# Kernel optimization log

Measured on AMD Instinct MI355X. Metric: run time of the kernel, lower is better.

The kernel has to match this reference:

```python
import jax, jax.numpy as jnp
import numpy as np

# Cross-attention fusion core (SpatialTransformer CrossAttention, LDM-style):
#   q = x @ Wq ; k = ctx @ Wk ; v = ctx @ Wv  (bias-free projections)
#   multi-head split, sim = q k^T * d_head**-0.5, softmax, out = attn v, merge heads, to_out.

N_HEADS = 2
D_HEAD = 32


def setup_inputs() -> dict:
    key = jax.random.key(0)
    ks = jax.random.split(key, 7)
    B, N, C = 8, 3136, 64           # batch=bs*num_key, tokens=H*W=56*56, snn channels
    Nc, Cc = 3136, 64               # ann context tokens / channels (resnet18 layer1)
    inner = N_HEADS * D_HEAD        # 64
    std = 0.02
    return {
        "x": jax.random.normal(ks[0], (B, N, C), jnp.float32),
        "context": jax.random.normal(ks[1], (B, Nc, Cc), jnp.float32),
        "Wq": std * jax.random.normal(ks[2], (C, inner), jnp.float32),
        "Wk": std * jax.random.normal(ks[3], (Cc, inner), jnp.float32),
        "Wv": std * jax.random.normal(ks[4], (Cc, inner), jnp.float32),
        "Wo": std * jax.random.normal(ks[5], (inner, C), jnp.float32),
        "bo": jnp.zeros((C,), jnp.float32),
    }


def reference(x, context, Wq, Wk, Wv, Wo, bo):
    B, N, C = x.shape
    H, D = N_HEADS, D_HEAD
    scale = D ** -0.5
    # projections -> [B, H, N, D]
    q = jnp.einsum('bnc,ci->bni', x, Wq).reshape(B, N, H, D).transpose(0, 2, 1, 3)
    k = jnp.einsum('bmc,ci->bmi', context, Wk).reshape(B, -1, H, D).transpose(0, 2, 1, 3)
    v = jnp.einsum('bmc,ci->bmi', context, Wv).reshape(B, -1, H, D).transpose(0, 2, 1, 3)
    # full attention matrix [B, H, N, Nc] (as in the original explicit-einsum impl)
    sim = jnp.einsum('bhid,bhjd->bhij', q, k) * scale
    attn = jax.nn.softmax(sim, axis=-1)
    out = jnp.einsum('bhij,bhjd->bhid', attn, v)
    out = out.transpose(0, 2, 1, 3).reshape(B, N, H * D)
    return jnp.einsum('bni,ic->bnc', out, Wo) + bo
```

## Files before the change

### kernel.cpp

```cpp
#include <hip/hip_runtime.h>
#include <hip/hip_bf16.h>


constexpr int Bc = 8;
constexpr int Nq = 3136;
constexpr int NT = 49;
constexpr size_t SEG   = (size_t)Bc * Nq * 64;
constexpr size_t OPOFF = 3 * SEG;
constexpr size_t LPOFF = OPOFF + (size_t)1176 * 4096;
constexpr size_t WS_NEED3 = (LPOFF + (size_t)1176 * 256) * 2;

typedef short bf16x8 __attribute__((ext_vector_type(8)));
typedef float f32x4  __attribute__((ext_vector_type(4)));

#define QSCALE (0.17677669529663687f * 1.4426950408889634f)

__device__ inline unsigned int f2bf(float f) {
    __hip_bfloat16 h = __float2bfloat16(f);
    unsigned short u;
    __builtin_memcpy(&u, &h, 2);
    return (unsigned int)u;
}

__device__ inline unsigned int cvtpk(float lo, float hi) {
    unsigned int r;
    asm("v_cvt_pk_bf16_f32 %0, %1, %2" : "=v"(r) : "v"(lo), "v"(hi));
    return r;
}

__device__ inline float exp2_hw(float x) { return __builtin_amdgcn_exp2f(x); }

#define GLOAD16(gp, lp)                                                        \
    __builtin_amdgcn_global_load_lds(                                          \
        (const __attribute__((address_space(1))) unsigned int*)(gp),           \
        (__attribute__((address_space(3))) unsigned int*)(lp), 16, 0, 0)

__global__ __launch_bounds__(256)
void proj_kernel(const float* __restrict__ x, const float* __restrict__ ctx,
                 const float* __restrict__ Wq, const float* __restrict__ Wk,
                 const float* __restrict__ Wv, unsigned short* __restrict__ ws) {
    __shared__ short Xls[128 * 72];
    __shared__ short Wtl[64 * 72];

    const int m = blockIdx.y;
    const float* in = (m == 0) ? x : ctx;
    const float* W  = (m == 0) ? Wq : (m == 1 ? Wk : Wv);
    const size_t row0 = (size_t)blockIdx.x * 128;
    const int tid = threadIdx.x;

    {
        const int k  = tid & 63;
        const int cb = tid >> 6;
        const float* wr = W + k * 64 + cb * 16;
        float4 w0 = *(const float4*)(wr + 0);
        float4 w1 = *(const float4*)(wr + 4);
        float4 w2 = *(const float4*)(wr + 8);
        float4 w3 = *(const float4*)(wr + 12);
        float wv[16] = {w0.x,w0.y,w0.z,w0.w, w1.x,w1.y,w1.z,w1.w,
                        w2.x,w2.y,w2.z,w2.w, w3.x,w3.y,w3.z,w3.w};
#pragma unroll
        for (int j = 0; j < 16; ++j)
            Wtl[(cb * 16 + j) * 72 + k] = (short)f2bf(wv[j]);
    }
    {
        const int r    = tid >> 1;
        const int half = tid & 1;
        const float* xr = in + (row0 + r) * 64 + half * 32;
        unsigned int u[16];
#pragma unroll
        for (int i = 0; i < 8; ++i) {
            float4 v = *(const float4*)(xr + 4 * i);
            u[2*i]   = f2bf(v.x) | (f2bf(v.y) << 16);
            u[2*i+1] = f2bf(v.z) | (f2bf(v.w) << 16);
        }
        char* dst = (char*)Xls + r * 144 + half * 64;
#pragma unroll
        for (int c = 0; c < 4; ++c)
            *(uint4*)(dst + 16 * c) = make_uint4(u[4*c], u[4*c+1], u[4*c+2], u[4*c+3]);
    }
    __syncthreads();

    const int lane = tid & 63;
    const int w    = tid >> 6;
    const int l15  = lane & 15;
    const int g    = lane >> 4;

    f32x4 acc[2][4];
#pragma unroll
    for (int ti = 0; ti < 2; ++ti)
#pragma unroll
        for (int tc = 0; tc < 4; ++tc) acc[ti][tc] = (f32x4){0.f,0.f,0.f,0.f};

#pragma unroll
    for (int kk = 0; kk < 2; ++kk) {
#pragma unroll
        for (int ti = 0; ti < 2; ++ti) {
            const int T = 2 * w + ti;
            bf16x8 a = *(const bf16x8*)((char*)Xls + (16 * T + l15) * 144 + kk * 64 + 16 * g);
#pragma unroll
            for (int tc = 0; tc < 4; ++tc) {
                bf16x8 bfr = *(const bf16x8*)((char*)Wtl + (16 * tc + l15) * 144 + kk * 64 + 16 * g);
                acc[ti][tc] = __builtin_amdgcn_mfma_f32_16x16x32_bf16(a, bfr, acc[ti][tc], 0, 0, 0);
            }
        }
    }

    unsigned short* Qs = ws;
    char* Ktc = (char*)(ws + SEG);
    char* Vtc = (char*)(ws + 2 * SEG);

#pragma unroll
    for (int ti = 0; ti < 2; ++ti) {
#pragma unroll
        for (int tc = 0; tc < 4; ++tc) {
            const int col = 16 * tc + l15;
            if (m == 0) {
#pragma unroll
                for (int r = 0; r < 4; ++r) {
                    const size_t grow = row0 + 32 * w + 16 * ti + 4 * g + r;
                    Qs[grow * 64 + col] = (unsigned short)f2bf(acc[ti][tc][r] * QSCALE);
                }
            } else if (m == 1) {
#pragma unroll
                for (int r = 0; r < 4; ++r) {
                    const size_t grow = row0 + 32 * w + 16 * ti + 4 * g + r;
                    const size_t tile = grow >> 6;
                    const int key = (int)(grow & 63);
                    const int off = (key * 128 + col * 2) ^ ((key & 7) << 4);
                    *(unsigned short*)(Ktc + tile * 8192 + off) =
                        (unsigned short)f2bf(acc[ti][tc][r]);
                }
            } else {
                const size_t grow0 = row0 + 32 * w + 16 * ti + 4 * g;
                const size_t tile = grow0 >> 6;
                const int key0 = (int)(grow0 & 63);
                const int off = (col * 128 + key0 * 2) ^ ((col & 15) << 3);
                uint2 pv;
                pv.x = f2bf(acc[ti][tc][0]) | (f2bf(acc[ti][tc][1]) << 16);
                pv.y = f2bf(acc[ti][tc][2]) | (f2bf(acc[ti][tc][3]) << 16);
                *(uint2*)(Vtc + tile * 8192 + off) = pv;
            }
        }
    }
}

__global__ __launch_bounds__(256)
void flash_kernel(unsigned short* __restrict__ ws, int P) {
    __shared__ __align__(16) char pool[32768];
    char* Kpool = pool;
    char* Vpool = pool + 16384;

    const int tid   = threadIdx.x;
    const int lane  = tid & 63;
    const int w     = tid >> 6;
    const int h     = w & 1;
    const int half  = w >> 1;
    const int l15   = lane & 15;
    const int g     = lane >> 4;
    const int bid   = blockIdx.x;
    const int b     = bid & 7;
    const int idx   = bid >> 3;
    const int qt    = idx / P;
    const int part  = idx - qt * P;
    const int q0    = qt * 64;
    const int base  = NT / P, rem = NT - base * P;
    const int t0    = part * base + (part < rem ? part : rem);
    const int tend  = t0 + base + (part < rem ? 1 : 0);

    const unsigned short* Qs = ws;
    const char* Ktb = (const char*)(ws + SEG)     + (size_t)b * NT * 8192;
    const char* Vtb = (const char*)(ws + 2 * SEG) + (size_t)b * NT * 8192;

    const unsigned short* qp0 =
        Qs + ((size_t)(b * Nq + q0 + half * 32 + l15)) * 64 + h * 32 + g * 8;
    const bf16x8 qf0 = *(const bf16x8*)qp0;
    const bf16x8 qf1 = *(const bf16x8*)(qp0 + 16 * 64);

    const int koff  = (l15 * 128 + h * 64 + g * 16) ^ ((l15 & 7) << 4);
    const int vrowA = (h * 32 + l15) * 128;
    const int vsw   = l15 << 3;
    const int stoff = tid * 16;

    union VF { bf16x8 v; unsigned int u[4]; };
    VF ones;
    ones.u[0] = 0x3F803F80u; ones.u[1] = 0x3F803F80u;
    ones.u[2] = 0x3F803F80u; ones.u[3] = 0x3F803F80u;

    f32x4 oacc00 = {0.f,0.f,0.f,0.f};
    f32x4 oacc01 = {0.f,0.f,0.f,0.f};
    f32x4 oacc10 = {0.f,0.f,0.f,0.f};
    f32x4 oacc11 = {0.f,0.f,0.f,0.f};
    f32x4 ls0    = {0.f,0.f,0.f,0.f};
    f32x4 ls1    = {0.f,0.f,0.f,0.f};

#pragma unroll
    for (int i = 0; i < 2; ++i) {
        const char* ks = Ktb + (size_t)(t0 + i) * 8192;
        const char* vs = Vtb + (size_t)(t0 + i) * 8192;
        GLOAD16(ks + stoff,        Kpool + i * 8192 + stoff);
        GLOAD16(ks + stoff + 4096, Kpool + i * 8192 + stoff + 4096);
        GLOAD16(vs + stoff,        Vpool + i * 8192 + stoff);
        GLOAD16(vs + stoff + 4096, Vpool + i * 8192 + stoff + 4096);
    }
    asm volatile("s_waitcnt vmcnt(4)" ::: "memory");
    __builtin_amdgcn_s_barrier();
    __builtin_amdgcn_sched_barrier(0);

#pragma unroll 1
    for (int t = t0; t < tend; ++t) {
        const int cb = (t - t0) & 1;
        const char* Kb = Kpool + cb * 8192;
        const char* Vb = Vpool + cb * 8192;

        __builtin_amdgcn_s_setprio(1);
        bf16x8 kA0 = *(const bf16x8*)(Kb + koff);
        bf16x8 kA1 = *(const bf16x8*)(Kb + 2048 + koff);
        bf16x8 kB0 = *(const bf16x8*)(Kb + 4096 + koff);
        bf16x8 kB1 = *(const bf16x8*)(Kb + 4096 + 2048 + koff);
        uint2 vA00 = *(const uint2*)(Vb + ((vrowA +       8 * g) ^ vsw));
        uint2 vA01 = *(const uint2*)(Vb + ((vrowA + 32 +  8 * g) ^ vsw));
        uint2 vA10 = *(const uint2*)(Vb + ((vrowA + 2048 +      8 * g) ^ vsw));
        uint2 vA11 = *(const uint2*)(Vb + ((vrowA + 2048 + 32 + 8 * g) ^ vsw));
        uint2 vB00 = *(const uint2*)(Vb + ((vrowA + 64 +      8 * g) ^ vsw));
        uint2 vB01 = *(const uint2*)(Vb + ((vrowA + 64 + 32 + 8 * g) ^ vsw));
        uint2 vB10 = *(const uint2*)(Vb + ((vrowA + 2048 + 64 +      8 * g) ^ vsw));
        uint2 vB11 = *(const uint2*)(Vb + ((vrowA + 2048 + 64 + 32 + 8 * g) ^ vsw));

#define CHUNK(kf0, kf1, v00, v01, v10, v11)                                     \
        {                                                                       \
            f32x4 s0a = __builtin_amdgcn_mfma_f32_16x16x32_bf16(kf0, qf0, (f32x4){0.f,0.f,0.f,0.f}, 0, 0, 0); \
            f32x4 s1a = __builtin_amdgcn_mfma_f32_16x16x32_bf16(kf1, qf0, (f32x4){0.f,0.f,0.f,0.f}, 0, 0, 0); \
            f32x4 s0b = __builtin_amdgcn_mfma_f32_16x16x32_bf16(kf0, qf1, (f32x4){0.f,0.f,0.f,0.f}, 0, 0, 0); \
            f32x4 s1b = __builtin_amdgcn_mfma_f32_16x16x32_bf16(kf1, qf1, (f32x4){0.f,0.f,0.f,0.f}, 0, 0, 0); \
            float pa0 = exp2_hw(s0a[0]), pa1 = exp2_hw(s0a[1]);                 \
            float pa2 = exp2_hw(s0a[2]), pa3 = exp2_hw(s0a[3]);                 \
            float pa4 = exp2_hw(s1a[0]), pa5 = exp2_hw(s1a[1]);                 \
            float pa6 = exp2_hw(s1a[2]), pa7 = exp2_hw(s1a[3]);                 \
            float pb0 = exp2_hw(s0b[0]), pb1 = exp2_hw(s0b[1]);                 \
            float pb2 = exp2_hw(s0b[2]), pb3 = exp2_hw(s0b[3]);                 \
            float pb4 = exp2_hw(s1b[0]), pb5 = exp2_hw(s1b[1]);                 \
            float pb6 = exp2_hw(s1b[2]), pb7 = exp2_hw(s1b[3]);                 \
            VF af0, af1;                                                        \
            af0.u[0] = cvtpk(pa0, pa1); af0.u[1] = cvtpk(pa2, pa3);             \
            af0.u[2] = cvtpk(pa4, pa5); af0.u[3] = cvtpk(pa6, pa7);             \
            af1.u[0] = cvtpk(pb0, pb1); af1.u[1] = cvtpk(pb2, pb3);             \
            af1.u[2] = cvtpk(pb4, pb5); af1.u[3] = cvtpk(pb6, pb7);             \
            VF vfA, vfB;                                                        \
            vfA.u[0] = v00.x; vfA.u[1] = v00.y; vfA.u[2] = v01.x; vfA.u[3] = v01.y; \
            vfB.u[0] = v10.x; vfB.u[1] = v10.y; vfB.u[2] = v11.x; vfB.u[3] = v11.y; \
            oacc00 = __builtin_amdgcn_mfma_f32_16x16x32_bf16(af0.v, vfA.v, oacc00, 0, 0, 0); \
            oacc01 = __builtin_amdgcn_mfma_f32_16x16x32_bf16(af0.v, vfB.v, oacc01, 0, 0, 0); \
            oacc10 = __builtin_amdgcn_mfma_f32_16x16x32_bf16(af1.v, vfA.v, oacc10, 0, 0, 0); \
            oacc11 = __builtin_amdgcn_mfma_f32_16x16x32_bf16(af1.v, vfB.v, oacc11, 0, 0, 0); \
            ls0    = __builtin_amdgcn_mfma_f32_16x16x32_bf16(af0.v, ones.v, ls0, 0, 0, 0);   \
            ls1    = __builtin_amdgcn_mfma_f32_16x16x32_bf16(af1.v, ones.v, ls1, 0, 0, 0);   \
        }

        CHUNK(kA0, kA1, vA00, vA01, vA10, vA11)
        CHUNK(kB0, kB1, vB00, vB01, vB10, vB11)
#undef CHUNK
        __builtin_amdgcn_s_setprio(0);

        if (t + 1 < tend) {
            __builtin_amdgcn_s_barrier();
            __builtin_amdgcn_sched_barrier(0);
            if (t + 2 < tend) {
                const char* ks = Ktb + (size_t)(t + 2) * 8192;
                const char* vs = Vtb + (size_t)(t + 2) * 8192;
                GLOAD16(ks + stoff,        Kb + stoff);
                GLOAD16(ks + stoff + 4096, Kb + stoff + 4096);
                GLOAD16(vs + stoff,        Vb + stoff);
                GLOAD16(vs + stoff + 4096, Vb + stoff + 4096);
                asm volatile("s_waitcnt vmcnt(4)" ::: "memory");
            } else {
                asm volatile("s_waitcnt vmcnt(0)" ::: "memory");
            }
            __builtin_amdgcn_s_barrier();
            __builtin_amdgcn_sched_barrier(0);
        }
    }

    float* lp = (float*)(ws + LPOFF) + (size_t)bid * 128;
    if (l15 == 0) {
#pragma unroll
        for (int r = 0; r < 4; ++r) {
            lp[h * 64 + half * 32 + 4 * g + r]      = ls0[r];
            lp[h * 64 + half * 32 + 16 + 4 * g + r] = ls1[r];
        }
    }

    _Float16* Op = (_Float16*)(ws + OPOFF) + (size_t)bid * 4096;
#pragma unroll
    for (int r = 0; r < 4; ++r) {
        const int q = half * 32 + 4 * g + r;
        Op[q * 64 + h * 32 + l15]             = (_Float16)oacc00[r];
        Op[q * 64 + h * 32 + 16 + l15]        = (_Float16)oacc01[r];
        Op[(q + 16) * 64 + h * 32 + l15]      = (_Float16)oacc10[r];
        Op[(q + 16) * 64 + h * 32 + 16 + l15] = (_Float16)oacc11[r];
    }
}

__global__ __launch_bounds__(256)
void combine_kernel(const unsigned short* __restrict__ ws, const float* __restrict__ Wo,
                    const float* __restrict__ bo, float* __restrict__ out, int P) {
    __shared__ short As[64 * 72];
    __shared__ short Wtl[64 * 72];

    const int tid = threadIdx.x;
    const int cid = blockIdx.x;
    const int b   = cid & 7;
    const int qt  = cid >> 3;
    const int q0  = qt * 64;

    const int bid0 = ((qt * P) << 3) | b;

    {
        const int k  = tid & 63;
        const int cb = tid >> 6;
        const float* wr = Wo + k * 64 + cb * 16;
        float4 w0 = *(const float4*)(wr + 0);
        float4 w1 = *(const float4*)(wr + 4);
        float4 w2 = *(const float4*)(wr + 8);
        float4 w3 = *(const float4*)(wr + 12);
        float wv[16] = {w0.x,w0.y,w0.z,w0.w, w1.x,w1.y,w1.z,w1.w,
                        w2.x,w2.y,w2.z,w2.w, w3.x,w3.y,w3.z,w3.w};
#pragma unroll
        for (int j = 0; j < 16; ++j)
            Wtl[(cb * 16 + j) * 72 + k] = (short)f2bf(wv[j]);
    }

    {
        const int r  = tid >> 2;
        const int cg = (tid & 3) << 4;
        const int hh = cg >> 5;

        float lsum = 0.f;
        float o[16];
#pragma unroll
        for (int j = 0; j < 16; ++j) o[j] = 0.f;

        for (int p = 0; p < P; ++p) {
            const int pb = bid0 + 8 * p;
            const float* lpp = (const float*)(ws + LPOFF) + (size_t)pb * 128;
            lsum += lpp[hh * 64 + r];
            const _Float16* Opp = (const _Float16*)(ws + OPOFF) + (size_t)pb * 4096;
            union H4 { uint4 u; _Float16 h[8]; };
            H4 x0, x1;
            x0.u = *(const uint4*)(Opp + (size_t)r * 64 + cg);
            x1.u = *(const uint4*)(Opp + (size_t)r * 64 + cg + 8);
#pragma unroll
            for (int j = 0; j < 8; ++j) {
                o[j]     += (float)x0.h[j];
                o[j + 8] += (float)x1.h[j];
            }
        }
        const float inv = 1.0f / lsum;
        short* arow = As + r * 72 + cg;
#pragma unroll
        for (int j = 0; j < 16; ++j) arow[j] = (short)f2bf(o[j] * inv);
    }
    __syncthreads();

    const int lane = tid & 63;
    const int w    = tid >> 6;
    const int l15  = lane & 15;
    const int g    = lane >> 4;
#pragma unroll
    for (int tc = 0; tc < 4; ++tc) {
        const int col = 16 * tc + l15;
        const float bias = bo[col];
        f32x4 accE = {bias, bias, bias, bias};
#pragma unroll
        for (int kk = 0; kk < 2; ++kk) {
            bf16x8 a   = *(const bf16x8*)((char*)As  + (16 * w + l15) * 144 + kk * 64 + 16 * g);
            bf16x8 bfr = *(const bf16x8*)((char*)Wtl + col * 144 + kk * 64 + 16 * g);
            accE = __builtin_amdgcn_mfma_f32_16x16x32_bf16(a, bfr, accE, 0, 0, 0);
        }
        float* ob = out + ((size_t)(b * Nq + q0 + 16 * w + 4 * g)) * 64 + col;
#pragma unroll
        for (int r = 0; r < 4; ++r) ob[(size_t)r * 64] = accE[r];
    }
}

extern "C" void kernel_launch(void* const* d_in, const int* in_sizes, int n_in,
                              void* d_out, int out_size, void* d_ws, size_t ws_size,
                              hipStream_t stream) {
    const float* x   = (const float*)d_in[0];
    const float* ctx = (const float*)d_in[1];
    const float* Wq  = (const float*)d_in[2];
    const float* Wk  = (const float*)d_in[3];
    const float* Wv  = (const float*)d_in[4];
    const float* Wo  = (const float*)d_in[5];
    const float* bo  = (const float*)d_in[6];
    float* out = (float*)d_out;
    unsigned short* ws = (unsigned short*)d_ws;

    const int P = (ws_size >= WS_NEED3) ? 3 : 2;

    dim3 gproj(Bc * Nq / 128, 3);
    proj_kernel<<<gproj, 256, 0, stream>>>(x, ctx, Wq, Wk, Wv, ws);

    flash_kernel<<<dim3(Nq / 64 * Bc * P), 256, 0, stream>>>(ws, P);

    combine_kernel<<<dim3(Nq / 64 * Bc), 256, 0, stream>>>(ws, Wo, bo, out, P);
}
```

Measured before the change: 57.41 us.

## Switch flash inner loop to 32x32x16 MFMA with VALU row sums

Replaces the 16x16x32 MFMA tiling in the attention loop with 32x32x16 bf16 MFMAs, so each wave computes a 32-key by 32-query score tile and a 32x32 output tile. The V tile layout written by the projection kernel is re-swizzled to match the new operand fragments. The softmax denominator is now accumulated with VALU adds plus a cross-half shuffle instead of extra MFMAs against a ones vector. This aims to cut MFMA issue count and per-tile LDS reads, at the cost of a larger 16-wide accumulator and dependence on the new swizzle being correct.

New measurement: 62.05 us. +8.1%, slower.

```diff
diff --git a/kernel.cpp b/kernel.cpp
--- a/kernel.cpp
+++ b/kernel.cpp
@@ -12,6 +12,8 @@
 
 typedef short bf16x8 __attribute__((ext_vector_type(8)));
 typedef float f32x4  __attribute__((ext_vector_type(4)));
+typedef float f32x16 __attribute__((ext_vector_type(16)));
+typedef float f32x2  __attribute__((ext_vector_type(2)));
 
 #define QSCALE (0.17677669529663687f * 1.4426950408889634f)
 
@@ -134,7 +136,10 @@
                 const size_t grow0 = row0 + 32 * w + 16 * ti + 4 * g;
                 const size_t tile = grow0 >> 6;
                 const int key0 = (int)(grow0 & 63);
-                const int off = (col * 128 + key0 * 2) ^ ((col & 15) << 3);
+                const int kb = (key0 >> 2) & 3;
+                const int sb = ((kb & 1) << 1) | (kb >> 1);
+                const int off = (col * 128 + (key0 >> 4) * 32 + sb * 8)
+                                ^ ((col & 7) << 4);
                 uint2 pv;
                 pv.x = f2bf(acc[ti][tc][0]) | (f2bf(acc[ti][tc][1]) << 16);
                 pv.y = f2bf(acc[ti][tc][2]) | (f2bf(acc[ti][tc][3]) << 16);
@@ -150,48 +155,47 @@
     char* Kpool = pool;
     char* Vpool = pool + 16384;
 
-    const int tid   = threadIdx.x;
-    const int lane  = tid & 63;
-    const int w     = tid >> 6;
-    const int h     = w & 1;
-    const int half  = w >> 1;
-    const int l15   = lane & 15;
-    const int g     = lane >> 4;
-    const int bid   = blockIdx.x;
-    const int b     = bid & 7;
-    const int idx   = bid >> 3;
-    const int qt    = idx / P;
-    const int part  = idx - qt * P;
-    const int q0    = qt * 64;
-    const int base  = NT / P, rem = NT - base * P;
-    const int t0    = part * base + (part < rem ? part : rem);
-    const int tend  = t0 + base + (part < rem ? 1 : 0);
-
-    const unsigned short* Qs = ws;
+    const int tid  = threadIdx.x;
+    const int lane = tid & 63;
+    const int w    = tid >> 6;
+    const int h    = w & 1;
+    const int half = w >> 1;
+    const int l31  = lane & 31;
+    const int hi   = lane >> 5;
+    const int bid  = blockIdx.x;
+    const int b    = bid & 7;
+    const int idx  = bid >> 3;
+    const int qt   = idx / P;
+    const int part = idx - qt * P;
+    const int q0   = qt * 64;
+    const int base = NT / P, rem = NT - base * P;
+    const int t0   = part * base + (part < rem ? part : rem);
+    const int tend = t0 + base + (part < rem ? 1 : 0);
+
     const char* Ktb = (const char*)(ws + SEG)     + (size_t)b * NT * 8192;
     const char* Vtb = (const char*)(ws + 2 * SEG) + (size_t)b * NT * 8192;
 
-    const unsigned short* qp0 =
-        Qs + ((size_t)(b * Nq + q0 + half * 32 + l15)) * 64 + h * 32 + g * 8;
-    const bf16x8 qf0 = *(const bf16x8*)qp0;
-    const bf16x8 qf1 = *(const bf16x8*)(qp0 + 16 * 64);
-
-    const int koff  = (l15 * 128 + h * 64 + g * 16) ^ ((l15 & 7) << 4);
-    const int vrowA = (h * 32 + l15) * 128;
-    const int vsw   = l15 << 3;
+    const unsigned short* qrow =
+        ws + ((size_t)(b * Nq + q0 + half * 32 + l31)) * 64 + h * 32 + hi * 8;
+    const bf16x8 qf0 = *(const bf16x8*)qrow;
+    const bf16x8 qf1 = *(const bf16x8*)(qrow + 16);
+
+    const int sw    = (l31 & 7) << 4;
+    const int koff0 = l31 * 128 + ((h * 64 +      hi * 16) ^ sw);
+    const int koff1 = l31 * 128 + ((h * 64 + 32 + hi * 16) ^ sw);
+    const int vrow  = (h * 32 + l31) * 128;
+    int vg[4];
+#pragma unroll
+    for (int m2 = 0; m2 < 4; ++m2) vg[m2] = (m2 * 32 + hi * 16) ^ sw;
     const int stoff = tid * 16;
 
     union VF { bf16x8 v; unsigned int u[4]; };
-    VF ones;
-    ones.u[0] = 0x3F803F80u; ones.u[1] = 0x3F803F80u;
-    ones.u[2] = 0x3F803F80u; ones.u[3] = 0x3F803F80u;
-
-    f32x4 oacc00 = {0.f,0.f,0.f,0.f};
-    f32x4 oacc01 = {0.f,0.f,0.f,0.f};
-    f32x4 oacc10 = {0.f,0.f,0.f,0.f};
-    f32x4 oacc11 = {0.f,0.f,0.f,0.f};
-    f32x4 ls0    = {0.f,0.f,0.f,0.f};
-    f32x4 ls1    = {0.f,0.f,0.f,0.f};
+
+    f32x16 oacc = {0.f,0.f,0.f,0.f,0.f,0.f,0.f,0.f,
+                   0.f,0.f,0.f,0.f,0.f,0.f,0.f,0.f};
+    f32x2 lacc = {0.f, 0.f};
+    const f32x16 Z16 = {0.f,0.f,0.f,0.f,0.f,0.f,0.f,0.f,
+                        0.f,0.f,0.f,0.f,0.f,0.f,0.f,0.f};
 
 #pragma unroll
     for (int i = 0; i < 2; ++i) {
@@ -213,52 +217,35 @@
         const char* Vb = Vpool + cb * 8192;
 
         __builtin_amdgcn_s_setprio(1);
-        bf16x8 kA0 = *(const bf16x8*)(Kb + koff);
-        bf16x8 kA1 = *(const bf16x8*)(Kb + 2048 + koff);
-        bf16x8 kB0 = *(const bf16x8*)(Kb + 4096 + koff);
-        bf16x8 kB1 = *(const bf16x8*)(Kb + 4096 + 2048 + koff);
-        uint2 vA00 = *(const uint2*)(Vb + ((vrowA +       8 * g) ^ vsw));
-        uint2 vA01 = *(const uint2*)(Vb + ((vrowA + 32 +  8 * g) ^ vsw));
-        uint2 vA10 = *(const uint2*)(Vb + ((vrowA + 2048 +      8 * g) ^ vsw));
-        uint2 vA11 = *(const uint2*)(Vb + ((vrowA + 2048 + 32 + 8 * g) ^ vsw));
-        uint2 vB00 = *(const uint2*)(Vb + ((vrowA + 64 +      8 * g) ^ vsw));
-        uint2 vB01 = *(const uint2*)(Vb + ((vrowA + 64 + 32 + 8 * g) ^ vsw));
-        uint2 vB10 = *(const uint2*)(Vb + ((vrowA + 2048 + 64 +      8 * g) ^ vsw));
-        uint2 vB11 = *(const uint2*)(Vb + ((vrowA + 2048 + 64 + 32 + 8 * g) ^ vsw));
-
-#define CHUNK(kf0, kf1, v00, v01, v10, v11)                                     \
-        {                                                                       \
-            f32x4 s0a = __builtin_amdgcn_mfma_f32_16x16x32_bf16(kf0, qf0, (f32x4){0.f,0.f,0.f,0.f}, 0, 0, 0); \
-            f32x4 s1a = __builtin_amdgcn_mfma_f32_16x16x32_bf16(kf1, qf0, (f32x4){0.f,0.f,0.f,0.f}, 0, 0, 0); \
-            f32x4 s0b = __builtin_amdgcn_mfma_f32_16x16x32_bf16(kf0, qf1, (f32x4){0.f,0.f,0.f,0.f}, 0, 0, 0); \
-            f32x4 s1b = __builtin_amdgcn_mfma_f32_16x16x32_bf16(kf1, qf1, (f32x4){0.f,0.f,0.f,0.f}, 0, 0, 0); \
-            float pa0 = exp2_hw(s0a[0]), pa1 = exp2_hw(s0a[1]);                 \
-            float pa2 = exp2_hw(s0a[2]), pa3 = exp2_hw(s0a[3]);                 \
-            float pa4 = exp2_hw(s1a[0]), pa5 = exp2_hw(s1a[1]);                 \
-            float pa6 = exp2_hw(s1a[2]), pa7 = exp2_hw(s1a[3]);                 \
-            float pb0 = exp2_hw(s0b[0]), pb1 = exp2_hw(s0b[1]);                 \
-            float pb2 = exp2_hw(s0b[2]), pb3 = exp2_hw(s0b[3]);                 \
-            float pb4 = exp2_hw(s1b[0]), pb5 = exp2_hw(s1b[1]);                 \
-            float pb6 = exp2_hw(s1b[2]), pb7 = exp2_hw(s1b[3]);                 \
-            VF af0, af1;                                                        \
-            af0.u[0] = cvtpk(pa0, pa1); af0.u[1] = cvtpk(pa2, pa3);             \
-            af0.u[2] = cvtpk(pa4, pa5); af0.u[3] = cvtpk(pa6, pa7);             \
-            af1.u[0] = cvtpk(pb0, pb1); af1.u[1] = cvtpk(pb2, pb3);             \
-            af1.u[2] = cvtpk(pb4, pb5); af1.u[3] = cvtpk(pb6, pb7);             \
-            VF vfA, vfB;                                                        \
-            vfA.u[0] = v00.x; vfA.u[1] = v00.y; vfA.u[2] = v01.x; vfA.u[3] = v01.y; \
-            vfB.u[0] = v10.x; vfB.u[1] = v10.y; vfB.u[2] = v11.x; vfB.u[3] = v11.y; \
-            oacc00 = __builtin_amdgcn_mfma_f32_16x16x32_bf16(af0.v, vfA.v, oacc00, 0, 0, 0); \
-            oacc01 = __builtin_amdgcn_mfma_f32_16x16x32_bf16(af0.v, vfB.v, oacc01, 0, 0, 0); \
-            oacc10 = __builtin_amdgcn_mfma_f32_16x16x32_bf16(af1.v, vfA.v, oacc10, 0, 0, 0); \
-            oacc11 = __builtin_amdgcn_mfma_f32_16x16x32_bf16(af1.v, vfB.v, oacc11, 0, 0, 0); \
-            ls0    = __builtin_amdgcn_mfma_f32_16x16x32_bf16(af0.v, ones.v, ls0, 0, 0, 0);   \
-            ls1    = __builtin_amdgcn_mfma_f32_16x16x32_bf16(af1.v, ones.v, ls1, 0, 0, 0);   \
-        }
-
-        CHUNK(kA0, kA1, vA00, vA01, vA10, vA11)
-        CHUNK(kB0, kB1, vB00, vB01, vB10, vB11)
-#undef CHUNK
+#pragma unroll
+        for (int c2 = 0; c2 < 2; ++c2) {
+            bf16x8 k0 = *(const bf16x8*)(Kb + c2 * 4096 + koff0);
+            bf16x8 k1 = *(const bf16x8*)(Kb + c2 * 4096 + koff1);
+
+            f32x16 s = __builtin_amdgcn_mfma_f32_32x32x16_bf16(k0, qf0, Z16, 0, 0, 0);
+            s = __builtin_amdgcn_mfma_f32_32x32x16_bf16(k1, qf1, s, 0, 0, 0);
+
+            float p[16];
+#pragma unroll
+            for (int i = 0; i < 16; ++i) p[i] = exp2_hw(s[i]);
+
+            lacc += (f32x2){p[0], p[1]};   lacc += (f32x2){p[2], p[3]};
+            lacc += (f32x2){p[4], p[5]};   lacc += (f32x2){p[6], p[7]};
+            lacc += (f32x2){p[8], p[9]};   lacc += (f32x2){p[10], p[11]};
+            lacc += (f32x2){p[12], p[13]}; lacc += (f32x2){p[14], p[15]};
+
+            VF a0, a1;
+            a0.u[0] = cvtpk(p[0], p[1]);   a0.u[1] = cvtpk(p[2], p[3]);
+            a0.u[2] = cvtpk(p[4], p[5]);   a0.u[3] = cvtpk(p[6], p[7]);
+            a1.u[0] = cvtpk(p[8], p[9]);   a1.u[1] = cvtpk(p[10], p[11]);
+            a1.u[2] = cvtpk(p[12], p[13]); a1.u[3] = cvtpk(p[14], p[15]);
+
+            bf16x8 v0 = *(const bf16x8*)(Vb + vrow + vg[2 * c2]);
+            bf16x8 v1 = *(const bf16x8*)(Vb + vrow + vg[2 * c2 + 1]);
+
+            oacc = __builtin_amdgcn_mfma_f32_32x32x16_bf16(a0.v, v0, oacc, 0, 0, 0);
+            oacc = __builtin_amdgcn_mfma_f32_32x32x16_bf16(a1.v, v1, oacc, 0, 0, 0);
+        }
         __builtin_amdgcn_s_setprio(0);
 
         if (t + 1 < tend) {
@@ -280,23 +267,16 @@
         }
     }
 
+    float lsum = lacc[0] + lacc[1];
+    lsum += __shfl_xor(lsum, 32);
     float* lp = (float*)(ws + LPOFF) + (size_t)bid * 128;
-    if (l15 == 0) {
-#pragma unroll
-        for (int r = 0; r < 4; ++r) {
-            lp[h * 64 + half * 32 + 4 * g + r]      = ls0[r];
-            lp[h * 64 + half * 32 + 16 + 4 * g + r] = ls1[r];
-        }
-    }
+    if (hi == 0) lp[h * 64 + half * 32 + l31] = lsum;
 
     _Float16* Op = (_Float16*)(ws + OPOFF) + (size_t)bid * 4096;
 #pragma unroll
-    for (int r = 0; r < 4; ++r) {
-        const int q = half * 32 + 4 * g + r;
-        Op[q * 64 + h * 32 + l15]             = (_Float16)oacc00[r];
-        Op[q * 64 + h * 32 + 16 + l15]        = (_Float16)oacc01[r];
-        Op[(q + 16) * 64 + h * 32 + l15]      = (_Float16)oacc10[r];
-        Op[(q + 16) * 64 + h * 32 + 16 + l15] = (_Float16)oacc11[r];
+    for (int r = 0; r < 16; ++r) {
+        const int q = half * 32 + (r & 3) + 8 * (r >> 2) + 4 * hi;
+        Op[q * 64 + h * 32 + l31] = (_Float16)oacc[r];
     }
 }
 
```
